# Optimization experiments

Measured on AMD Instinct MI355X. Metric: run time of the kernel, lower is better.

## Reference

```python
import jax, jax.numpy as jnp
import numpy as np

N = 50000      # nodes
E = 800000     # edges (avg degree 16)
IN_DIM = 256
HID = 64
HEADS = 4
OUT_DIM = 128
NEG_SLOPE = 0.2


def setup_inputs() -> dict:
    key = jax.random.key(0)
    ks = jax.random.split(key, 9)
    h = jax.random.normal(ks[0], (N, IN_DIM), jnp.float32)
    src = jax.random.randint(ks[1], (E,), 0, N, dtype=jnp.int32)
    dst = jax.random.randint(ks[2], (E,), 0, N, dtype=jnp.int32)
    # layer1: fc IN_DIM -> HEADS*HID, attn vectors [HEADS, HID]
    W1 = jax.random.normal(ks[3], (IN_DIM, HEADS * HID), jnp.float32) * (1.0 / np.sqrt(IN_DIM))
    attn_l1 = jax.random.normal(ks[4], (HEADS, HID), jnp.float32) * (1.0 / np.sqrt(HID))
    attn_r1 = jax.random.normal(ks[5], (HEADS, HID), jnp.float32) * (1.0 / np.sqrt(HID))
    # layer2: fc HEADS*HID -> 1*OUT_DIM, attn vectors [1, OUT_DIM]
    W2 = jax.random.normal(ks[6], (HEADS * HID, OUT_DIM), jnp.float32) * (1.0 / np.sqrt(HEADS * HID))
    attn_l2 = jax.random.normal(ks[7], (1, OUT_DIM), jnp.float32) * (1.0 / np.sqrt(OUT_DIM))
    attn_r2 = jax.random.normal(ks[8], (1, OUT_DIM), jnp.float32) * (1.0 / np.sqrt(OUT_DIM))
    return {"h": h, "src": src, "dst": dst,
            "W1": W1, "attn_l1": attn_l1, "attn_r1": attn_r1,
            "W2": W2, "attn_l2": attn_l2, "attn_r2": attn_r2}


def _gat_conv(h, W, attn_l, attn_r, src, dst):
    """DGL-style GATConv: returns [N, heads, out_dim]."""
    H, D = attn_l.shape
    feat = (h @ W).reshape(-1, H, D)                       # [N, H, D]
    el = jnp.einsum('nhd,hd->nh', feat, attn_l)            # [N, H]
    er = jnp.einsum('nhd,hd->nh', feat, attn_r)            # [N, H]
    e = jax.nn.leaky_relu(el[src] + er[dst], NEG_SLOPE)    # [E, H]
    # edge softmax over incoming edges of each dst node (stable)
    emax = jax.lax.stop_gradient(
        jax.ops.segment_max(e, dst, num_segments=N))       # [N, H]
    ex = jnp.exp(e - emax[dst])                            # [E, H]
    denom = jax.ops.segment_sum(ex, dst, num_segments=N)   # [N, H]
    alpha = ex / denom[dst]                                # [E, H]
    msg = alpha[:, :, None] * feat[src]                    # [E, H, D]
    return jax.ops.segment_sum(msg, dst, num_segments=N)   # [N, H, D]


def reference(h, src, dst, W1, attn_l1, attn_r1, W2, attn_l2, attn_r2):
    h1 = _gat_conv(h, W1, attn_l1, attn_r1, src, dst)      # [N, HEADS, HID]
    h1 = jax.nn.elu(h1.reshape(N, HEADS * HID))            # view + ELU
    h2 = _gat_conv(h1, W2, attn_l2, attn_r2, src, dst)     # [N, 1, OUT_DIM]
    return h2.squeeze(1)                                   # [N, OUT_DIM]
```

## Files before the change

kernel.cpp:

```cpp
#include <hip/hip_runtime.h>
#include <hip/hip_bf16.h>
#include <hip/hip_fp16.h>
#include <math.h>

#define NN 50000
#define EE 800000

__device__ __forceinline__ float lrelu(float v){ return v > 0.f ? v : 0.2f * v; }
__device__ __forceinline__ float sel4(float4 v, int h){
  return h == 0 ? v.x : h == 1 ? v.y : h == 2 ? v.z : v.w;
}
__device__ __forceinline__ ushort f2bf(float x){
  union { __hip_bfloat16 b; ushort u; } cv; cv.b = __float2bfloat16(x); return cv.u;
}
__device__ __forceinline__ float bf2f(ushort u){
  union { uint u; float f; } cv; cv.u = (uint)u << 16; return cv.f;
}
__device__ __forceinline__ ushort f2h(float x){
  union { __half h; ushort u; } cv; cv.h = __float2half(x); return cv.u;
}
__device__ __forceinline__ float bflo(uint u){ union{uint u; float f;} c; c.u = u << 16; return c.f; }
__device__ __forceinline__ float bfhi(uint u){ union{uint u; float f;} c; c.u = u & 0xffff0000u; return c.f; }
__device__ __forceinline__ float hlo(uint u){
  union{ ushort us; __half h; } c; c.us = (ushort)(u & 0xffffu); return __half2float(c.h);
}
__device__ __forceinline__ float hhi(uint u){
  union{ ushort us; __half h; } c; c.us = (ushort)(u >> 16); return __half2float(c.h);
}

typedef __attribute__((ext_vector_type(8))) short bf16x8;
typedef __attribute__((ext_vector_type(4))) float f32x4;

__device__ __forceinline__ void gload16(const ushort* g, ushort* l){
  const auto* gp = reinterpret_cast<const __attribute__((address_space(1))) ushort*>((size_t)g);
  auto* lp = reinterpret_cast<__attribute__((address_space(3))) ushort*>((size_t)l);
  __builtin_amdgcn_global_load_lds(gp, lp, 16, 0, 0);
}

__global__ void k_hist(const int* __restrict__ dst, int* __restrict__ cnt, int E){
  int i = blockIdx.x * blockDim.x + threadIdx.x;
  if (i < E) atomicAdd(&cnt[dst[i]], 1);
}

__global__ __launch_bounds__(1024) void k_scan_bsum(const int* __restrict__ cnt, int* __restrict__ bsum, int n){
  __shared__ int ws[16];
  int t = threadIdx.x, i = blockIdx.x*1024 + t;
  int v = (i < n) ? cnt[i] : 0;
  #pragma unroll
  for (int off = 32; off; off >>= 1) v += __shfl_down(v, off);
  if ((t & 63) == 0) ws[t >> 6] = v;
  __syncthreads();
  if (t < 64){
    int x = (t < 16) ? ws[t] : 0;
    #pragma unroll
    for (int off = 32; off; off >>= 1) x += __shfl_down(x, off);
    if (t == 0) bsum[blockIdx.x] = x;
  }
}

__global__ void k_scan_boff(const int* __restrict__ bsum, int* __restrict__ boff,
                            int nb, int* __restrict__ rowptr, int n){
  int t = threadIdx.x;
  int v = (t < nb) ? bsum[t] : 0;
  int x = v;
  #pragma unroll
  for (int off = 1; off < 64; off <<= 1){ int y = __shfl_up(x, off); if (t >= off) x += y; }
  if (t < nb) boff[t] = x - v;
  if (t == 63) rowptr[n] = x;
}

__global__ __launch_bounds__(1024) void k_scan_write(const int* __restrict__ cnt, const int* __restrict__ boff,
                                                     int* __restrict__ rowptr, int* __restrict__ cursor, int n){
  __shared__ int ws[16];
  int t = threadIdx.x, w = t >> 6, lane = t & 63, i = blockIdx.x*1024 + t;
  int v = (i < n) ? cnt[i] : 0;
  int x = v;
  #pragma unroll
  for (int off = 1; off < 64; off <<= 1){ int y = __shfl_up(x, off); if (lane >= off) x += y; }
  if (lane == 63) ws[w] = x;
  __syncthreads();
  if (t < 16){
    int y = ws[t];
    #pragma unroll
    for (int off = 1; off < 16; off <<= 1){ int z = __shfl_up(y, off); if (t >= off) y += z; }
    ws[t] = y;
  }
  __syncthreads();
  if (i < n){
    int ex = boff[blockIdx.x] + ((w > 0) ? ws[w-1] : 0) + x - v;
    rowptr[i] = ex;
    cursor[i] = ex;
  }
}

__global__ void k_scatter(const int* __restrict__ src, const int* __restrict__ dst,
                          int* __restrict__ cursor, int* __restrict__ csr_src, int E){
  int i = blockIdx.x * blockDim.x + threadIdx.x;
  if (i < E){ int p = atomicAdd(&cursor[dst[i]], 1); csr_src[p] = src[i]; }
}

__global__ void k_prep(const float* __restrict__ A, ushort* __restrict__ Ab,
                       const float* __restrict__ W1, ushort* __restrict__ Bth1, ushort* __restrict__ Btl1,
                       const float* __restrict__ W2, ushort* __restrict__ Bth2, ushort* __restrict__ Btl2){
  int b = blockIdx.x, t = threadIdx.x;
  if (b < 12500){
    int i = b*256 + t;
    float4 v = ((const float4*)A)[i];
    ((ushort4*)Ab)[i] = make_ushort4(f2bf(v.x), f2bf(v.y), f2bf(v.z), f2bf(v.w));
  } else if (b < 12756){
    int k = b - 12500;
    float x = W1[(size_t)k*256 + t];
    ushort h = f2bf(x);
    Bth1[(size_t)t*256 + k] = h;
    Btl1[(size_t)t*256 + k] = f2bf(x - bf2f(h));
  } else {
    int k = b - 12756;
    if (t < 128){
      float x = W2[(size_t)k*128 + t];
      ushort h = f2bf(x);
      Bth2[(size_t)t*256 + k] = h;
      Btl2[(size_t)t*256 + k] = f2bf(x - bf2f(h));
    }
  }
}

template<int MODE>
__global__ __launch_bounds__(512, 4) void k_mgemm(
    const ushort* __restrict__ Ab,
    const ushort* __restrict__ Bth, const ushort* __restrict__ Btl,
    void* __restrict__ Cout, const float* __restrict__ avl, const float* __restrict__ avr,
    float* __restrict__ el, float* __restrict__ er, int M, int K, int N)
{
  __shared__ __align__(16) ushort sA[2][128*32];
  __shared__ __align__(16) ushort sBh[2][128*32];
  __shared__ __align__(16) ushort sBl[2][128*32];
  __shared__ float sEL[2][128], sER[2][128];
  int tid = threadIdx.x;
  int w = tid >> 6, lane = tid & 63;
  int bm = blockIdx.y*128, bn = blockIdx.x*128;
  int wm = (w & 3)*32, wn = (w >> 2)*64;
  int fr = lane & 15, fg = lane >> 4;

  int srow = 16*w + (lane >> 2);
  int skoff = (lane & 3)*8;
  int arow = bm + srow; if (arow > M-1) arow = M-1;
  const ushort* gA  = Ab  + (size_t)arow*K + skoff;
  const ushort* gBh = Bth + (size_t)(bn + srow)*K + skoff;
  const ushort* gBl = Btl + (size_t)(bn + srow)*K + skoff;
  int lslice = 16*w*32;

  const int nk = K >> 5;
  gload16(gA,  &sA[0][lslice]);
  gload16(gBh, &sBh[0][lslice]);
  gload16(gBl, &sBl[0][lslice]);
  __syncthreads();

  f32x4 acc[2][4] = {};
  for (int kt = 0; kt < nk; ++kt){
    int buf = kt & 1;
    if (kt + 1 < nk){
      int k1 = (kt + 1) << 5;
      gload16(gA + k1,  &sA[buf^1][lslice]);
      gload16(gBh + k1, &sBh[buf^1][lslice]);
      gload16(gBl + k1, &sBl[buf^1][lslice]);
    }
    bf16x8 ah[2], bh[4], bl[4];
    #pragma unroll
    for (int ti = 0; ti < 2; ++ti)
      ah[ti] = *(const bf16x8*)&sA[buf][(wm + ti*16 + fr)*32 + fg*8];
    #pragma unroll
    for (int tj = 0; tj < 4; ++tj){
      int bi = (wn + tj*16 + fr)*32 + fg*8;
      bh[tj] = *(const bf16x8*)&sBh[buf][bi];
      bl[tj] = *(const bf16x8*)&sBl[buf][bi];
    }
    #pragma unroll
    for (int ti = 0; ti < 2; ++ti)
      #pragma unroll
      for (int tj = 0; tj < 4; ++tj){
        acc[ti][tj] = __builtin_amdgcn_mfma_f32_16x16x32_bf16(ah[ti], bh[tj], acc[ti][tj], 0,0,0);
        acc[ti][tj] = __builtin_amdgcn_mfma_f32_16x16x32_bf16(ah[ti], bl[tj], acc[ti][tj], 0,0,0);
      }
    __syncthreads();
  }

  int colhead = bn + wn;
  float wl[4], wr[4];
  #pragma unroll
  for (int tj = 0; tj < 4; ++tj){
    int c = colhead + tj*16 + fr;
    wl[tj] = avl[c]; wr[tj] = avr[c];
  }
  #pragma unroll
  for (int ti = 0; ti < 2; ++ti)
    #pragma unroll
    for (int i = 0; i < 4; ++i){
      int row = bm + wm + ti*16 + fg*4 + i;
      float pl = 0.f, pr = 0.f;
      #pragma unroll
      for (int tj = 0; tj < 4; ++tj){
        float v = acc[ti][tj][i];
        pl = fmaf(v, wl[tj], pl);
        pr = fmaf(v, wr[tj], pr);
        if (row < M){
          int col = colhead + tj*16 + fr;
          if (MODE == 1) ((ushort*)Cout)[(size_t)row*256 + col] = f2bf(v);
          else           ((ushort*)Cout)[(size_t)row*128 + col] = f2h(v);
        }
      }
      #pragma unroll
      for (int mk = 1; mk < 16; mk <<= 1){
        pl += __shfl_xor(pl, mk);
        pr += __shfl_xor(pr, mk);
      }
      if (fr == 0){
        if (MODE == 1){
          if (row < M){ el[row*4 + (colhead >> 6)] = pl; er[row*4 + (colhead >> 6)] = pr; }
        } else {
          int lr = wm + ti*16 + fg*4 + i;
          sEL[w >> 2][lr] = pl; sER[w >> 2][lr] = pr;
        }
      }
    }
  if (MODE == 2){
    __syncthreads();
    if (tid < 128){
      int row = bm + tid;
      if (row < M){
        el[row] = sEL[0][tid] + sEL[1][tid];
        er[row] = sER[0][tid] + sER[1][tid];
      }
    }
  }
}

__global__ __launch_bounds__(256) void k_fused1(
    const int* __restrict__ rowptr, const int* __restrict__ csr_src,
    const float* __restrict__ el, const float* __restrict__ er,
    const ushort* __restrict__ featb, ushort* __restrict__ h1b)
{
  __shared__ __align__(16) float p_sh[4][64*4];
  __shared__ int si_sh[4][64];
  int w = threadIdx.x >> 6, lane = threadIdx.x & 63;
  int n = blockIdx.x*4 + w;
  if (n >= NN) return;
  int b = rowptr[n], deg = rowptr[n+1] - b;
  int l32 = lane & 31, half = lane >> 5;
  int h = l32 >> 3;
  float4 er4 = *(const float4*)&er[n*4];
  float4 s4 = make_float4(0,0,0,0);
  float acc[8] = {0.f,0.f,0.f,0.f,0.f,0.f,0.f,0.f};

  for (int c0 = 0; c0 < deg; c0 += 64){
    int C = min(64, deg - c0);
    int si = 0;
    float4 p4 = make_float4(0,0,0,0);
    if (lane < C){
      si = csr_src[b + c0 + lane];
      float4 l4 = *(const float4*)&el[si*4];
      p4.x = __expf(lrelu(l4.x + er4.x));
      p4.y = __expf(lrelu(l4.y + er4.y));
      p4.z = __expf(lrelu(l4.z + er4.z));
      p4.w = __expf(lrelu(l4.w + er4.w));
    }
    s4.x += p4.x; s4.y += p4.y; s4.z += p4.z; s4.w += p4.w;
    *(float4*)&p_sh[w][lane*4] = p4;
    si_sh[w][lane] = si;
    #pragma unroll 4
    for (int j = 0; j < C; j += 2){
      int e = j + half;
      float a = p_sh[w][e*4 + h];
      int sj = si_sh[w][e];
      uint4 u = *(const uint4*)&featb[(size_t)sj*256 + l32*8];
      acc[0] = fmaf(a, bflo(u.x), acc[0]); acc[1] = fmaf(a, bfhi(u.x), acc[1]);
      acc[2] = fmaf(a, bflo(u.y), acc[2]); acc[3] = fmaf(a, bfhi(u.y), acc[3]);
      acc[4] = fmaf(a, bflo(u.z), acc[4]); acc[5] = fmaf(a, bfhi(u.z), acc[5]);
      acc[6] = fmaf(a, bflo(u.w), acc[6]); acc[7] = fmaf(a, bfhi(u.w), acc[7]);
    }
  }
  #pragma unroll
  for (int k = 0; k < 8; ++k) acc[k] += __shfl_xor(acc[k], 32);
  #pragma unroll
  for (int off = 32; off; off >>= 1){
    s4.x += __shfl_xor(s4.x, off); s4.y += __shfl_xor(s4.y, off);
    s4.z += __shfl_xor(s4.z, off); s4.w += __shfl_xor(s4.w, off);
  }
  if (lane < 32){
    float rs = (deg > 0) ? 1.0f / sel4(s4, h) : 0.f;
    ushort ob[8];
    #pragma unroll
    for (int k = 0; k < 8; ++k){
      float v = acc[k] * rs;
      v = (v > 0.f) ? v : expm1f(v);
      ob[k] = f2bf(v);
    }
    uint4 pk;
    pk.x = (uint)ob[0] | ((uint)ob[1] << 16);
    pk.y = (uint)ob[2] | ((uint)ob[3] << 16);
    pk.z = (uint)ob[4] | ((uint)ob[5] << 16);
    pk.w = (uint)ob[6] | ((uint)ob[7] << 16);
    *(uint4*)&h1b[(size_t)n*256 + l32*8] = pk;
  }
}

__global__ __launch_bounds__(256) void k_fused2(
    const int* __restrict__ rowptr, const int* __restrict__ csr_src,
    const float* __restrict__ el, const float* __restrict__ er,
    const ushort* __restrict__ featH, float* __restrict__ out)
{
  __shared__ float p_sh[4][64];
  __shared__ int si_sh[4][64];
  int w = threadIdx.x >> 6, lane = threadIdx.x & 63;
  int n = blockIdx.x*4 + w;
  if (n >= NN) return;
  int b = rowptr[n], deg = rowptr[n+1] - b;
  int l16 = lane & 15, grp = lane >> 4;
  float er_n = er[n];
  float s = 0.f;
  float acc[8] = {0.f,0.f,0.f,0.f,0.f,0.f,0.f,0.f};

  for (int c0 = 0; c0 < deg; c0 += 64){
    int C = min(64, deg - c0);
    int si = 0;
    float p = 0.f;
    if (lane < C){
      si = csr_src[b + c0 + lane];
      p = __expf(lrelu(el[si] + er_n));
    }
    s += p;
    p_sh[w][lane] = p;
    si_sh[w][lane] = si;
    #pragma unroll 4
    for (int j = 0; j < C; j += 4){
      int e = j + grp;
      float a = p_sh[w][e];
      int sj = si_sh[w][e];
      uint4 u = *(const uint4*)&featH[(size_t)sj*128 + l16*8];
      acc[0] = fmaf(a, hlo(u.x), acc[0]); acc[1] = fmaf(a, hhi(u.x), acc[1]);
      acc[2] = fmaf(a, hlo(u.y), acc[2]); acc[3] = fmaf(a, hhi(u.y), acc[3]);
      acc[4] = fmaf(a, hlo(u.z), acc[4]); acc[5] = fmaf(a, hhi(u.z), acc[5]);
      acc[6] = fmaf(a, hlo(u.w), acc[6]); acc[7] = fmaf(a, hhi(u.w), acc[7]);
    }
  }
  #pragma unroll
  for (int k = 0; k < 8; ++k){
    acc[k] += __shfl_xor(acc[k], 16);
    acc[k] += __shfl_xor(acc[k], 32);
  }
  #pragma unroll
  for (int off = 32; off; off >>= 1) s += __shfl_xor(s, off);
  if (lane < 16){
    float rs = (deg > 0) ? 1.0f / s : 0.f;
    float4 o0 = make_float4(acc[0]*rs, acc[1]*rs, acc[2]*rs, acc[3]*rs);
    float4 o1 = make_float4(acc[4]*rs, acc[5]*rs, acc[6]*rs, acc[7]*rs);
    *(float4*)&out[(size_t)n*128 + l16*8]     = o0;
    *(float4*)&out[(size_t)n*128 + l16*8 + 4] = o1;
  }
}

static inline size_t align256(size_t x){ return (x + 255) & ~(size_t)255; }

extern "C" void kernel_launch(void* const* d_in, const int* in_sizes, int n_in,
                              void* d_out, int out_size, void* d_ws, size_t ws_size,
                              hipStream_t stream){
  const float* h_in = (const float*)d_in[0];
  const int*   src  = (const int*)d_in[1];
  const int*   dst  = (const int*)d_in[2];
  const float* W1   = (const float*)d_in[3];
  const float* al1  = (const float*)d_in[4];
  const float* ar1  = (const float*)d_in[5];
  const float* W2   = (const float*)d_in[6];
  const float* al2  = (const float*)d_in[7];
  const float* ar2  = (const float*)d_in[8];
  float* out = (float*)d_out;

  char* ws = (char*)d_ws;
  size_t off = 0;
  ushort* Ab     = (ushort*)(ws + off); off = align256(off + (size_t)NN*256*2);
  ushort* featb  = (ushort*)(ws + off); off = align256(off + (size_t)NN*256*2);
  ushort* feat2  = (ushort*)(ws + off); off = align256(off + (size_t)NN*128*2);
  float* el1     = (float*)(ws + off);  off = align256(off + (size_t)NN*4*4);
  float* er1     = (float*)(ws + off);  off = align256(off + (size_t)NN*4*4);
  int* rowptr    = (int*)(ws + off);    off = align256(off + (size_t)(NN+1)*4);
  int* cnt       = (int*)(ws + off);    off = align256(off + (size_t)NN*4);
  int* cursor    = (int*)(ws + off);    off = align256(off + (size_t)NN*4);
  int* csr_src   = (int*)(ws + off);    off = align256(off + (size_t)EE*4);
  ushort* Bth1   = (ushort*)(ws + off); off = align256(off + (size_t)256*256*2);
  ushort* Btl1   = (ushort*)(ws + off); off = align256(off + (size_t)256*256*2);
  ushort* Bth2   = (ushort*)(ws + off); off = align256(off + (size_t)128*256*2);
  ushort* Btl2   = (ushort*)(ws + off); off = align256(off + (size_t)128*256*2);
  int* bsum      = (int*)(ws + off);    off = align256(off + (size_t)64*4);
  int* boff      = (int*)(ws + off);    off = align256(off + (size_t)64*4);
  if (off > ws_size) return;

  ushort* h1b = Ab;
  float* el2 = el1;
  float* er2 = er1;

  const int EB = (EE + 255)/256;
  const int FB = (NN + 3)/4;
  const int NB = (NN + 1023)/1024;
  const int MT = (NN + 127)/128;

  hipMemsetAsync(cnt, 0, (size_t)NN*4, stream);
  k_hist<<<EB, 256, 0, stream>>>(dst, cnt, EE);
  k_scan_bsum<<<NB, 1024, 0, stream>>>(cnt, bsum, NN);
  k_scan_boff<<<1, 64, 0, stream>>>(bsum, boff, NB, rowptr, NN);
  k_scan_write<<<NB, 1024, 0, stream>>>(cnt, boff, rowptr, cursor, NN);
  k_scatter<<<EB, 256, 0, stream>>>(src, dst, cursor, csr_src, EE);

  k_prep<<<13012, 256, 0, stream>>>(h_in, Ab, W1, Bth1, Btl1, W2, Bth2, Btl2);

  k_mgemm<1><<<dim3(2, MT), 512, 0, stream>>>(Ab, Bth1, Btl1, featb, al1, ar1, el1, er1, NN, 256, 256);
  k_fused1<<<FB, 256, 0, stream>>>(rowptr, csr_src, el1, er1, featb, h1b);

  k_mgemm<2><<<dim3(1, MT), 512, 0, stream>>>(h1b, Bth2, Btl2, feat2, al2, ar2, el2, er2, NN, 256, 128);
  k_fused2<<<FB, 256, 0, stream>>>(rowptr, csr_src, el2, er2, feat2, out);
}
```

Before: 254.5 us.

## Merge histogram into prep kernel and use packed FMA in aggregation loops

The edge-degree histogram is folded into the prep kernel as extra blocks, which removes one kernel launch. Both aggregation kernels now accumulate with inline-asm v_pk_fma_f32 on float2 pairs and unroll the edge loop further. The ELU path uses __expf(v)-1 in place of expm1f, which loses some accuracy for small negative values. The volatile asm may stop the compiler from scheduling around the FMAs, and the extra unroll raises register pressure.

```diff
diff --git a/kernel.cpp b/kernel.cpp
--- a/kernel.cpp
+++ b/kernel.cpp
@@ -27,6 +27,9 @@
 __device__ __forceinline__ float hhi(uint u){
   union{ ushort us; __half h; } c; c.us = (ushort)(u >> 16); return __half2float(c.h);
 }
+__device__ __forceinline__ void pkfma(float2 &acc, float2 f, float2 a){
+  asm volatile("v_pk_fma_f32 %0, %1, %2, %0" : "+v"(acc) : "v"(f), "v"(a));
+}
 
 typedef __attribute__((ext_vector_type(8))) short bf16x8;
 typedef __attribute__((ext_vector_type(4))) float f32x4;
@@ -35,11 +38,6 @@
   const auto* gp = reinterpret_cast<const __attribute__((address_space(1))) ushort*>((size_t)g);
   auto* lp = reinterpret_cast<__attribute__((address_space(3))) ushort*>((size_t)l);
   __builtin_amdgcn_global_load_lds(gp, lp, 16, 0, 0);
-}
-
-__global__ void k_hist(const int* __restrict__ dst, int* __restrict__ cnt, int E){
-  int i = blockIdx.x * blockDim.x + threadIdx.x;
-  if (i < E) atomicAdd(&cnt[dst[i]], 1);
 }
 
 __global__ __launch_bounds__(1024) void k_scan_bsum(const int* __restrict__ cnt, int* __restrict__ bsum, int n){
@@ -101,7 +99,8 @@
 
 __global__ void k_prep(const float* __restrict__ A, ushort* __restrict__ Ab,
                        const float* __restrict__ W1, ushort* __restrict__ Bth1, ushort* __restrict__ Btl1,
-                       const float* __restrict__ W2, ushort* __restrict__ Bth2, ushort* __restrict__ Btl2){
+                       const float* __restrict__ W2, ushort* __restrict__ Bth2, ushort* __restrict__ Btl2,
+                       const int* __restrict__ dst, int* __restrict__ cnt){
   int b = blockIdx.x, t = threadIdx.x;
   if (b < 12500){
     int i = b*256 + t;
@@ -113,7 +112,7 @@
     ushort h = f2bf(x);
     Bth1[(size_t)t*256 + k] = h;
     Btl1[(size_t)t*256 + k] = f2bf(x - bf2f(h));
-  } else {
+  } else if (b < 13012){
     int k = b - 12756;
     if (t < 128){
       float x = W2[(size_t)k*128 + t];
@@ -121,6 +120,9 @@
       Bth2[(size_t)t*256 + k] = h;
       Btl2[(size_t)t*256 + k] = f2bf(x - bf2f(h));
     }
+  } else {
+    int i = (b - 13012)*256 + t;
+    atomicAdd(&cnt[dst[i]], 1);
   }
 }
 
@@ -249,7 +251,7 @@
   int h = l32 >> 3;
   float4 er4 = *(const float4*)&er[n*4];
   float4 s4 = make_float4(0,0,0,0);
-  float acc[8] = {0.f,0.f,0.f,0.f,0.f,0.f,0.f,0.f};
+  float2 a0 = make_float2(0.f,0.f), a1 = a0, a2 = a0, a3 = a0;
 
   for (int c0 = 0; c0 < deg; c0 += 64){
     int C = min(64, deg - c0);
@@ -266,20 +268,23 @@
     s4.x += p4.x; s4.y += p4.y; s4.z += p4.z; s4.w += p4.w;
     *(float4*)&p_sh[w][lane*4] = p4;
     si_sh[w][lane] = si;
-    #pragma unroll 4
+    #pragma unroll 8
     for (int j = 0; j < C; j += 2){
       int e = j + half;
       float a = p_sh[w][e*4 + h];
       int sj = si_sh[w][e];
       uint4 u = *(const uint4*)&featb[(size_t)sj*256 + l32*8];
-      acc[0] = fmaf(a, bflo(u.x), acc[0]); acc[1] = fmaf(a, bfhi(u.x), acc[1]);
-      acc[2] = fmaf(a, bflo(u.y), acc[2]); acc[3] = fmaf(a, bfhi(u.y), acc[3]);
-      acc[4] = fmaf(a, bflo(u.z), acc[4]); acc[5] = fmaf(a, bfhi(u.z), acc[5]);
-      acc[6] = fmaf(a, bflo(u.w), acc[6]); acc[7] = fmaf(a, bfhi(u.w), acc[7]);
-    }
-  }
-  #pragma unroll
-  for (int k = 0; k < 8; ++k) acc[k] += __shfl_xor(acc[k], 32);
+      float2 aa = make_float2(a, a);
+      pkfma(a0, make_float2(bflo(u.x), bfhi(u.x)), aa);
+      pkfma(a1, make_float2(bflo(u.y), bfhi(u.y)), aa);
+      pkfma(a2, make_float2(bflo(u.z), bfhi(u.z)), aa);
+      pkfma(a3, make_float2(bflo(u.w), bfhi(u.w)), aa);
+    }
+  }
+  a0.x += __shfl_xor(a0.x, 32); a0.y += __shfl_xor(a0.y, 32);
+  a1.x += __shfl_xor(a1.x, 32); a1.y += __shfl_xor(a1.y, 32);
+  a2.x += __shfl_xor(a2.x, 32); a2.y += __shfl_xor(a2.y, 32);
+  a3.x += __shfl_xor(a3.x, 32); a3.y += __shfl_xor(a3.y, 32);
   #pragma unroll
   for (int off = 32; off; off >>= 1){
     s4.x += __shfl_xor(s4.x, off); s4.y += __shfl_xor(s4.y, off);
@@ -287,11 +292,12 @@
   }
   if (lane < 32){
     float rs = (deg > 0) ? 1.0f / sel4(s4, h) : 0.f;
+    float vv[8] = {a0.x, a0.y, a1.x, a1.y, a2.x, a2.y, a3.x, a3.y};
     ushort ob[8];
     #pragma unroll
     for (int k = 0; k < 8; ++k){
-      float v = acc[k] * rs;
-      v = (v > 0.f) ? v : expm1f(v);
+      float v = vv[k] * rs;
+      v = (v > 0.f) ? v : (__expf(v) - 1.f);
       ob[k] = f2bf(v);
     }
     uint4 pk;
@@ -317,7 +323,7 @@
   int l16 = lane & 15, grp = lane >> 4;
   float er_n = er[n];
   float s = 0.f;
-  float acc[8] = {0.f,0.f,0.f,0.f,0.f,0.f,0.f,0.f};
+  float2 a0 = make_float2(0.f,0.f), a1 = a0, a2 = a0, a3 = a0;
 
   for (int c0 = 0; c0 < deg; c0 += 64){
     int C = min(64, deg - c0);
@@ -330,18 +336,20 @@
     s += p;
     p_sh[w][lane] = p;
     si_sh[w][lane] = si;
-    #pragma unroll 4
+    #pragma unroll 8
     for (int j = 0; j < C; j += 4){
       int e = j + grp;
       float a = p_sh[w][e];
       int sj = si_sh[w][e];
       uint4 u = *(const uint4*)&featH[(size_t)sj*128 + l16*8];
-      acc[0] = fmaf(a, hlo(u.x), acc[0]); acc[1] = fmaf(a, hhi(u.x), acc[1]);
-      acc[2] = fmaf(a, hlo(u.y), acc[2]); acc[3] = fmaf(a, hhi(u.y), acc[3]);
-      acc[4] = fmaf(a, hlo(u.z), acc[4]); acc[5] = fmaf(a, hhi(u.z), acc[5]);
-      acc[6] = fmaf(a, hlo(u.w), acc[6]); acc[7] = fmaf(a, hhi(u.w), acc[7]);
-    }
-  }
+      float2 aa = make_float2(a, a);
+      pkfma(a0, make_float2(hlo(u.x), hhi(u.x)), aa);
+      pkfma(a1, make_float2(hlo(u.y), hhi(u.y)), aa);
+      pkfma(a2, make_float2(hlo(u.z), hhi(u.z)), aa);
+      pkfma(a3, make_float2(hlo(u.w), hhi(u.w)), aa);
+    }
+  }
+  float acc[8] = {a0.x, a0.y, a1.x, a1.y, a2.x, a2.y, a3.x, a3.y};
   #pragma unroll
   for (int k = 0; k < 8; ++k){
     acc[k] += __shfl_xor(acc[k], 16);
@@ -403,14 +411,12 @@
   const int MT = (NN + 127)/128;
 
   hipMemsetAsync(cnt, 0, (size_t)NN*4, stream);
-  k_hist<<<EB, 256, 0, stream>>>(dst, cnt, EE);
+  k_prep<<<13012 + EB, 256, 0, stream>>>(h_in, Ab, W1, Bth1, Btl1, W2, Bth2, Btl2, dst, cnt);
   k_scan_bsum<<<NB, 1024, 0, stream>>>(cnt, bsum, NN);
   k_scan_boff<<<1, 64, 0, stream>>>(bsum, boff, NB, rowptr, NN);
   k_scan_write<<<NB, 1024, 0, stream>>>(cnt, boff, rowptr, cursor, NN);
   k_scatter<<<EB, 256, 0, stream>>>(src, dst, cursor, csr_src, EE);
 
-  k_prep<<<13012, 256, 0, stream>>>(h_in, Ab, W1, Bth1, Btl1, W2, Bth2, Btl2);
-
   k_mgemm<1><<<dim3(2, MT), 512, 0, stream>>>(Ab, Bth1, Btl1, featb, al1, ar1, el1, er1, NN, 256, 256);
   k_fused1<<<FB, 256, 0, stream>>>(rowptr, csr_src, el1, er1, featb, h1b);
 
```

New measurement: 247.1 us. 1.03x faster.
